# Performance work log

Hardware: AMD Instinct MI355X
Metric: run time of the kernel (lower is better)

Reference implementation:

```python
import jax, jax.numpy as jnp
import numpy as np

# Static group structure: B groups, each of uniform size N, feature dim C.
# (The torch module handles ragged groups with a Python loop; with uniform
# groups the pad-to-max step is an identity and the math below is exact.)
B, N, C = 512, 64, 1024
EPS = 1e-12  # F.normalize default eps


def setup_inputs() -> dict:
    key = jax.random.key(0)
    feats = jax.random.normal(key, (B * N, C), dtype=jnp.float32)
    # adjacent equal labels: group g occupies rows [g*N, (g+1)*N)
    labels = jnp.repeat(jnp.arange(B, dtype=jnp.int32), N)
    return {"feats": feats, "labels": labels}


def reference(feats, labels):
    # labels encode contiguous uniform groups of size N (see setup_inputs),
    # so grouping is a static reshape.
    g = feats.reshape(B, N, C)                                  # [B, N, C]
    # F.normalize(dim=1): row-wise L2 normalize with eps clamp
    norms = jnp.linalg.norm(g, axis=-1, keepdims=True)
    gn = g / jnp.maximum(norms, EPS)
    # per-group cosine-similarity matrix and mean relation score
    sim = jnp.einsum('bnc,bmc->bnm', gn, gn)                    # [B, N, N]
    rel = sim.mean(axis=2)                                      # [B, N]
    # argsort descending (torch.argsort(..., descending=True))
    order = jnp.argsort(-rel, axis=1)                           # [B, N]
    sorted_g = jnp.take_along_axis(g, order[:, :, None], axis=1)
    out_sorted = sorted_g.reshape(B, N * C)                     # [B, N*C]
    out_input = g.reshape(B, N * C)                             # input-order concat (training=True)
    return out_sorted, out_input
```

## Files before the change

### kernel.cpp

```cpp
#include <hip/hip_runtime.h>
#include <math.h>


constexpr int Bq = 512;
constexpr int Nq = 64;
constexpr int Cq = 1024;
constexpr int C4 = Cq / 4;
constexpr int G4 = Nq * C4;
constexpr int OUT_HALF4 = Bq * G4;

typedef float f4 __attribute__((ext_vector_type(4)));

__global__ __launch_bounds__(1024)
void group_sorter_kernel(const float* __restrict__ feats, float* __restrict__ out) {
    __shared__ double sp[4][C4][4];
    __shared__ float  s_lds[Cq];
    __shared__ double rnorm[Nq];
    __shared__ double rel[Nq];
    __shared__ int    dst_row[Nq];

    const int b    = blockIdx.x;
    const int t    = threadIdx.x;
    const int wave = t >> 6;
    const int lane = t & 63;

    const f4* __restrict__ g4 = reinterpret_cast<const f4*>(feats) + (size_t)b * G4;
    f4* __restrict__ os = reinterpret_cast<f4*>(out) + (size_t)b * G4;
    f4* __restrict__ oi = reinterpret_cast<f4*>(out) + OUT_HALF4 + (size_t)b * G4;

    for (int n = wave; n < Nq; n += 16) {
        const f4* row = g4 + n * C4;
        double acc = 0.0;
        #pragma unroll
        for (int j = 0; j < 4; ++j) {
            f4 v = row[lane + 64 * j];
            acc += (double)v.x * v.x + (double)v.y * v.y
                 + (double)v.z * v.z + (double)v.w * v.w;
        }
        #pragma unroll
        for (int off = 32; off > 0; off >>= 1) acc += __shfl_xor(acc, off, 64);
        if (lane == 0) rnorm[n] = 1.0 / fmax(sqrt(acc), 1e-12);
    }
    __syncthreads();

    {
        const int part = t >> 8;
        const int c4   = t & 255;
        double s0 = 0, s1 = 0, s2 = 0, s3 = 0;
        #pragma unroll 4
        for (int mm = 0; mm < 16; ++mm) {
            const int m = part * 16 + mm;
            f4 v = g4[m * C4 + c4];
            double rn = rnorm[m];
            s0 += (double)v.x * rn; s1 += (double)v.y * rn;
            s2 += (double)v.z * rn; s3 += (double)v.w * rn;
            __builtin_nontemporal_store(v, &oi[m * C4 + c4]);
        }
        sp[part][c4][0] = s0; sp[part][c4][1] = s1;
        sp[part][c4][2] = s2; sp[part][c4][3] = s3;
    }
    __syncthreads();
    {
        const int c4 = t >> 2, comp = t & 3;
        double sum = sp[0][c4][comp] + sp[1][c4][comp]
                   + sp[2][c4][comp] + sp[3][c4][comp];
        s_lds[c4 * 4 + comp] = (float)sum;
    }
    __syncthreads();

    {
        const f4* s4 = reinterpret_cast<const f4*>(s_lds);
        for (int n = wave; n < Nq; n += 16) {
            const f4* row = g4 + n * C4;
            double acc = 0.0;
            #pragma unroll
            for (int j = 0; j < 4; ++j) {
                f4 v  = row[lane + 64 * j];
                f4 sv = s4[lane + 64 * j];
                acc += (double)v.x * sv.x + (double)v.y * sv.y
                     + (double)v.z * sv.z + (double)v.w * sv.w;
            }
            #pragma unroll
            for (int off = 32; off > 0; off >>= 1) acc += __shfl_xor(acc, off, 64);
            if (lane == 0) rel[n] = acc * rnorm[n];
        }
    }
    __syncthreads();

    if (t < Nq) {
        double mine = rel[t];
        int r = 0;
        for (int m = 0; m < Nq; ++m) {
            double o = rel[m];
            r += (o > mine) || (o == mine && m < t);
        }
        dst_row[t] = r;
    }
    __syncthreads();

    {
        const int rsub = t >> 8;
        const int c4   = t & 255;
        #pragma unroll 4
        for (int i4 = 0; i4 < 16; ++i4) {
            const int i = i4 * 4 + rsub;
            f4 v = g4[i * C4 + c4];
            __builtin_nontemporal_store(v, &os[dst_row[i] * C4 + c4]);
        }
    }
}

extern "C" void kernel_launch(void* const* d_in, const int* in_sizes, int n_in,
                              void* d_out, int out_size, void* d_ws, size_t ws_size,
                              hipStream_t stream) {
    const float* feats = (const float*)d_in[0];
    float* out = (float*)d_out;
    hipLaunchKernelGGL(group_sorter_kernel, dim3(Bq), dim3(1024), 0, stream,
                       feats, out);
}
```

Before: 398.8 us.

## Keep each group's tile in registers and drop the repeated global reads

Each thread loads its 16 float4 values once into registers and reuses them for the norm pass, the column-sum pass, the relation dot products and the final scattered store. The earlier version re-read the group from global memory (or L2) four times. Row reductions now go through a wave shuffle plus a small cross-wave LDS reduction. This costs 64 extra VGPRs per thread at 1024 threads per block, which could cause spills or pressure, in exchange for less memory traffic.

```diff
diff --git a/kernel.cpp b/kernel.cpp
--- a/kernel.cpp
+++ b/kernel.cpp
@@ -14,6 +14,7 @@
 __global__ __launch_bounds__(1024)
 void group_sorter_kernel(const float* __restrict__ feats, float* __restrict__ out) {
     __shared__ double sp[4][C4][4];
+    __shared__ double red[4][16][4];
     __shared__ float  s_lds[Cq];
     __shared__ double rnorm[Nq];
     __shared__ double rel[Nq];
@@ -21,69 +22,80 @@
 
     const int b    = blockIdx.x;
     const int t    = threadIdx.x;
-    const int wave = t >> 6;
     const int lane = t & 63;
+    const int part = t >> 8;
+    const int w4   = (t >> 6) & 3;
+    const int c4   = t & 255;
 
     const f4* __restrict__ g4 = reinterpret_cast<const f4*>(feats) + (size_t)b * G4;
     f4* __restrict__ os = reinterpret_cast<f4*>(out) + (size_t)b * G4;
     f4* __restrict__ oi = reinterpret_cast<f4*>(out) + OUT_HALF4 + (size_t)b * G4;
 
-    for (int n = wave; n < Nq; n += 16) {
-        const f4* row = g4 + n * C4;
-        double acc = 0.0;
-        #pragma unroll
-        for (int j = 0; j < 4; ++j) {
-            f4 v = row[lane + 64 * j];
-            acc += (double)v.x * v.x + (double)v.y * v.y
-                 + (double)v.z * v.z + (double)v.w * v.w;
-        }
+    f4 v[16];
+
+    #pragma unroll
+    for (int mm = 0; mm < 16; ++mm) {
+        const int m = part * 16 + mm;
+        v[mm] = g4[m * C4 + c4];
+        __builtin_nontemporal_store(v[mm], &oi[m * C4 + c4]);
+    }
+
+    #pragma unroll
+    for (int mm = 0; mm < 16; ++mm) {
+        f4 x = v[mm];
+        double acc = (double)x.x * x.x + (double)x.y * x.y
+                   + (double)x.z * x.z + (double)x.w * x.w;
         #pragma unroll
         for (int off = 32; off > 0; off >>= 1) acc += __shfl_xor(acc, off, 64);
-        if (lane == 0) rnorm[n] = 1.0 / fmax(sqrt(acc), 1e-12);
+        if (lane == 0) red[part][mm][w4] = acc;
+    }
+    __syncthreads();
+    if (t < Nq) {
+        const int p = t >> 4, r = t & 15;
+        double s = red[p][r][0] + red[p][r][1] + red[p][r][2] + red[p][r][3];
+        rnorm[t] = 1.0 / fmax(sqrt(s), 1e-12);
     }
     __syncthreads();
 
     {
-        const int part = t >> 8;
-        const int c4   = t & 255;
         double s0 = 0, s1 = 0, s2 = 0, s3 = 0;
-        #pragma unroll 4
+        #pragma unroll
         for (int mm = 0; mm < 16; ++mm) {
-            const int m = part * 16 + mm;
-            f4 v = g4[m * C4 + c4];
-            double rn = rnorm[m];
-            s0 += (double)v.x * rn; s1 += (double)v.y * rn;
-            s2 += (double)v.z * rn; s3 += (double)v.w * rn;
-            __builtin_nontemporal_store(v, &oi[m * C4 + c4]);
+            f4 x = v[mm];
+            double rn = rnorm[part * 16 + mm];
+            s0 += (double)x.x * rn; s1 += (double)x.y * rn;
+            s2 += (double)x.z * rn; s3 += (double)x.w * rn;
         }
         sp[part][c4][0] = s0; sp[part][c4][1] = s1;
         sp[part][c4][2] = s2; sp[part][c4][3] = s3;
     }
     __syncthreads();
     {
-        const int c4 = t >> 2, comp = t & 3;
-        double sum = sp[0][c4][comp] + sp[1][c4][comp]
-                   + sp[2][c4][comp] + sp[3][c4][comp];
-        s_lds[c4 * 4 + comp] = (float)sum;
+        const int cc = t >> 2, comp = t & 3;
+        double sum = sp[0][cc][comp] + sp[1][cc][comp]
+                   + sp[2][cc][comp] + sp[3][cc][comp];
+        s_lds[cc * 4 + comp] = (float)sum;
     }
     __syncthreads();
 
     {
         const f4* s4 = reinterpret_cast<const f4*>(s_lds);
-        for (int n = wave; n < Nq; n += 16) {
-            const f4* row = g4 + n * C4;
-            double acc = 0.0;
+        f4 sv = s4[c4];
+        #pragma unroll
+        for (int mm = 0; mm < 16; ++mm) {
+            f4 x = v[mm];
+            double p = (double)x.x * sv.x + (double)x.y * sv.y
+                     + (double)x.z * sv.z + (double)x.w * sv.w;
             #pragma unroll
-            for (int j = 0; j < 4; ++j) {
-                f4 v  = row[lane + 64 * j];
-                f4 sv = s4[lane + 64 * j];
-                acc += (double)v.x * sv.x + (double)v.y * sv.y
-                     + (double)v.z * sv.z + (double)v.w * sv.w;
-            }
-            #pragma unroll
-            for (int off = 32; off > 0; off >>= 1) acc += __shfl_xor(acc, off, 64);
-            if (lane == 0) rel[n] = acc * rnorm[n];
+            for (int off = 32; off > 0; off >>= 1) p += __shfl_xor(p, off, 64);
+            if (lane == 0) red[part][mm][w4] = p;
         }
+    }
+    __syncthreads();
+    if (t < Nq) {
+        const int p = t >> 4, r = t & 15;
+        double s = red[p][r][0] + red[p][r][1] + red[p][r][2] + red[p][r][3];
+        rel[t] = s * rnorm[t];
     }
     __syncthreads();
 
@@ -98,15 +110,10 @@
     }
     __syncthreads();
 
-    {
-        const int rsub = t >> 8;
-        const int c4   = t & 255;
-        #pragma unroll 4
-        for (int i4 = 0; i4 < 16; ++i4) {
-            const int i = i4 * 4 + rsub;
-            f4 v = g4[i * C4 + c4];
-            __builtin_nontemporal_store(v, &os[dst_row[i] * C4 + c4]);
-        }
+    #pragma unroll
+    for (int mm = 0; mm < 16; ++mm) {
+        const int dr = dst_row[part * 16 + mm];
+        __builtin_nontemporal_store(v[mm], &os[dr * C4 + c4]);
     }
 }
 
```

New measurement: 380.7 us. 4.5% less time.
